# Optimization experiments

Hardware: AMD Instinct MI355X
Metric: run time of the kernel (lower is better)

The kernel has to match this reference:

```python
import jax, jax.numpy as jnp
import numpy as np

N_NODES = 50000
N_REL = 4
N_EDGES = 250000
IN_F, HID_F, OUT_F = 512, 512, 256


def setup_inputs() -> dict:
    key = jax.random.key(0)
    ks = jax.random.split(key, 9)
    x = jax.random.normal(ks[0], (N_NODES, IN_F), dtype=jnp.float32)
    edge_src = jax.random.randint(ks[1], (N_REL, N_EDGES), 0, N_NODES, dtype=jnp.int64)
    edge_dst = jax.random.randint(ks[2], (N_REL, N_EDGES), 0, N_NODES, dtype=jnp.int64)
    s1 = 1.0 / np.sqrt(IN_F)
    s2 = 1.0 / np.sqrt(HID_F)
    Wself1 = jax.random.normal(ks[3], (N_REL, IN_F, HID_F), dtype=jnp.float32) * s1
    Wneigh1 = jax.random.normal(ks[4], (N_REL, IN_F, HID_F), dtype=jnp.float32) * s1
    b1 = jnp.zeros((N_REL, HID_F), dtype=jnp.float32)
    Wself2 = jax.random.normal(ks[5], (N_REL, HID_F, OUT_F), dtype=jnp.float32) * s2
    Wneigh2 = jax.random.normal(ks[6], (N_REL, HID_F, OUT_F), dtype=jnp.float32) * s2
    b2 = jnp.zeros((N_REL, OUT_F), dtype=jnp.float32)
    return {"x": x, "Wself1": Wself1, "Wneigh1": Wneigh1, "b1": b1,
            "Wself2": Wself2, "Wneigh2": Wneigh2, "b2": b2,
            "edge_src": edge_src, "edge_dst": edge_dst}


def _hetero_sage_layer(h, Wself, Wneigh, b, edge_src, edge_dst):
    """HeteroGraphConv(sum) over per-relation SAGEConv(mean) layers.

    DGL SAGEConv(mean): out_r = h @ W_self_r + mean_in_neigh(h) @ W_neigh_r + b_r;
    zero-in-degree nodes get a zero neighbor term (divide by max(deg,1)).
    """
    n = h.shape[0]
    out = jnp.zeros((n, Wself.shape[-1]), dtype=h.dtype)
    for r in range(Wself.shape[0]):  # small fixed number of relations
        src, dst = edge_src[r], edge_dst[r]
        deg = jax.ops.segment_sum(jnp.ones(src.shape, dtype=h.dtype), dst, num_segments=n)
        neigh_sum = jax.ops.segment_sum(h[src], dst, num_segments=n)  # [n, d]
        neigh = neigh_sum / jnp.maximum(deg, 1.0)[:, None]
        out = out + h @ Wself[r] + neigh @ Wneigh[r] + b[r]
    return out


def reference(x, Wself1, Wneigh1, b1, Wself2, Wneigh2, b2, edge_src, edge_dst):
    h = _hetero_sage_layer(x, Wself1, Wneigh1, b1, edge_src, edge_dst)
    h = jax.nn.relu(h)
    return _hetero_sage_layer(h, Wself2, Wneigh2, b2, edge_src, edge_dst)
```

## Files before the change

### kernel.cpp

```cpp
#include <hip/hip_runtime.h>
#include <stdint.h>

#define NNODES 50000
#define NREL 4
#define NEDGES 250000
#define INF 512
#define HIDF 512
#define OUTF 256
#define KCAT 2560
#define SCANB 49

typedef unsigned short u16;
typedef u16 u16x8 __attribute__((ext_vector_type(8)));
typedef __bf16 bf16x8 __attribute__((ext_vector_type(8)));
typedef float f32x4 __attribute__((ext_vector_type(4)));

__device__ __forceinline__ float bf2f(u16 b) {
    unsigned u = ((unsigned)b) << 16;
    return __builtin_bit_cast(float, u);
}
__device__ __forceinline__ u16 f2bf(float f) {
    unsigned u = __builtin_bit_cast(unsigned, f);
    u = (u + 0x7fffu + ((u >> 16) & 1u)) >> 16;
    return (u16)u;
}

#define GLOAD_LDS16(gsrc, ldst)                                                  \
    __builtin_amdgcn_global_load_lds(                                            \
        (__attribute__((address_space(1))) void*)(gsrc),                         \
        (__attribute__((address_space(3))) void*)(ldst), 16, 0, 0)


__global__ void cast_bf16_kernel(const float* __restrict__ in, u16* __restrict__ out, long total) {
    long i = ((long)blockIdx.x * blockDim.x + threadIdx.x) * 8;
    long stride = (long)gridDim.x * blockDim.x * 8;
    for (; i + 7 < total; i += stride) {
        float4 v0 = *(const float4*)(in + i);
        float4 v1 = *(const float4*)(in + i + 4);
        u16x8 o;
        o[0] = f2bf(v0.x); o[1] = f2bf(v0.y); o[2] = f2bf(v0.z); o[3] = f2bf(v0.w);
        o[4] = f2bf(v1.x); o[5] = f2bf(v1.y); o[6] = f2bf(v1.z); o[7] = f2bf(v1.w);
        *(u16x8*)(out + i) = o;
    }
}

__global__ void prep_w_kernel(const float* __restrict__ Wself, const float* __restrict__ Wneigh,
                              u16* __restrict__ WT, int N) {
    int total = N * KCAT;
    for (int idx = blockIdx.x * blockDim.x + threadIdx.x; idx < total;
         idx += gridDim.x * blockDim.x) {
        int n = idx / KCAT;
        int kg = idx - n * KCAT;
        int s = kg >> 9;
        int k = kg & 511;
        float v;
        if (s == 0) {
            v = Wself[(size_t)k * N + n] + Wself[(size_t)(512 + k) * N + n] +
                Wself[(size_t)(1024 + k) * N + n] + Wself[(size_t)(1536 + k) * N + n];
        } else {
            v = Wneigh[((size_t)(s - 1) * 512 + k) * N + n];
        }
        WT[idx] = f2bf(v);
    }
}

__global__ void prep_bias_kernel(const float* __restrict__ b1, const float* __restrict__ b2,
                                 float* __restrict__ b1s, float* __restrict__ b2s) {
    int t = threadIdx.x;
    if (t < HIDF) b1s[t] = b1[t] + b1[HIDF + t] + b1[2 * HIDF + t] + b1[3 * HIDF + t];
    if (t < OUTF) b2s[t] = b2[t] + b2[OUTF + t] + b2[2 * OUTF + t] + b2[3 * OUTF + t];
}


__global__ void hist_kernel(const int* __restrict__ dst, int* __restrict__ deg) {
    int tot = NREL * NEDGES;
    for (int i = blockIdx.x * blockDim.x + threadIdx.x; i < tot; i += gridDim.x * blockDim.x) {
        int r = i / NEDGES;
        atomicAdd(&deg[r * NNODES + dst[i]], 1);
    }
}

__global__ __launch_bounds__(1024) void scan1_kernel(const int* __restrict__ deg,
                                                     int* __restrict__ rp, int* __restrict__ bsum) {
    int rel = blockIdx.x / SCANB, blk = blockIdx.x % SCANB;
    int i = blk * 1024 + threadIdx.x;
    int v = (i < NNODES) ? deg[rel * NNODES + i] : 0;
    __shared__ int wsum[16];
    int lane = threadIdx.x & 63, wid = threadIdx.x >> 6;
    int x = v;
#pragma unroll
    for (int off = 1; off < 64; off <<= 1) {
        int o = __shfl_up(x, off);
        if (lane >= off) x += o;
    }
    if (lane == 63) wsum[wid] = x;
    __syncthreads();
    if (wid == 0) {
        int s = (lane < 16) ? wsum[lane] : 0;
#pragma unroll
        for (int off = 1; off < 16; off <<= 1) {
            int o = __shfl_up(s, off);
            if (lane >= off) s += o;
        }
        if (lane < 16) wsum[lane] = s;
    }
    __syncthreads();
    int excl = (wid > 0 ? wsum[wid - 1] : 0) + x - v;
    if (i < NNODES) rp[rel * (NNODES + 1) + i] = excl;
    if (threadIdx.x == 1023) bsum[blockIdx.x] = excl + v;
}

__global__ void scan2_kernel(const int* __restrict__ bsum, int* __restrict__ bofs) {
    int r = threadIdx.x >> 6, lane = threadIdx.x & 63;
    int v = (lane < SCANB) ? bsum[r * SCANB + lane] : 0;
    int x = v;
#pragma unroll
    for (int off = 1; off < 64; off <<= 1) {
        int o = __shfl_up(x, off);
        if (lane >= off) x += o;
    }
    if (lane < SCANB) bofs[r * SCANB + lane] = x - v;
}

__global__ __launch_bounds__(1024) void scan3_kernel(int* __restrict__ rp, int* __restrict__ cur,
                                                     const int* __restrict__ bofs) {
    int rel = blockIdx.x / SCANB, blk = blockIdx.x % SCANB;
    int i = blk * 1024 + threadIdx.x;
    if (i < NNODES) {
        int v = rp[rel * (NNODES + 1) + i] + bofs[rel * SCANB + blk];
        rp[rel * (NNODES + 1) + i] = v;
        cur[rel * NNODES + i] = v;
        if (i == 0) rp[rel * (NNODES + 1) + NNODES] = NEDGES;
    }
}

__global__ void fill_kernel(const int* __restrict__ esrc, const int* __restrict__ edst,
                            int* __restrict__ cur, int* __restrict__ col) {
    int tot = NREL * NEDGES;
    for (int i = blockIdx.x * blockDim.x + threadIdx.x; i < tot; i += gridDim.x * blockDim.x) {
        int r = i / NEDGES;
        int d = edst[i];
        int pos = atomicAdd(&cur[r * NNODES + d], 1);
        col[r * NEDGES + pos] = esrc[i];
    }
}


__global__ __launch_bounds__(256) void aggregate_kernel(const u16* __restrict__ src,
                                                        const int* __restrict__ rp,
                                                        const int* __restrict__ col,
                                                        u16* __restrict__ out) {
    int node = blockIdx.x * 4 + (threadIdx.x >> 6);
    int rel = blockIdx.y;
    if (node >= NNODES) return;
    const int* r = rp + rel * (NNODES + 1);
    const int* cl = col + rel * NEDGES;
    int l = threadIdx.x & 63;
    int p0 = r[node], p1 = r[node + 1];
    float scale = (p1 > p0) ? 1.0f / (float)(p1 - p0) : 1.0f;
    float acc[8] = {0.f, 0.f, 0.f, 0.f, 0.f, 0.f, 0.f, 0.f};
    int e = p0;
    for (; e + 2 <= p1; e += 2) {
        int s0 = cl[e], s1 = cl[e + 1];
        u16x8 v0 = *(const u16x8*)(src + (size_t)s0 * 512 + l * 8);
        u16x8 v1 = *(const u16x8*)(src + (size_t)s1 * 512 + l * 8);
#pragma unroll
        for (int j = 0; j < 8; ++j) acc[j] += bf2f(v0[j]) + bf2f(v1[j]);
    }
    if (e < p1) {
        int s0 = cl[e];
        u16x8 v0 = *(const u16x8*)(src + (size_t)s0 * 512 + l * 8);
#pragma unroll
        for (int j = 0; j < 8; ++j) acc[j] += bf2f(v0[j]);
    }
    u16x8 o;
#pragma unroll
    for (int j = 0; j < 8; ++j) o[j] = f2bf(acc[j] * scale);
    *(u16x8*)(out + ((size_t)rel * NNODES + node) * 512 + l * 8) = o;
}


template <int N, int OUTMODE>
__global__ __launch_bounds__(256, 4) void gemm_kernel(
    const u16* __restrict__ A0, const u16* __restrict__ A1, const u16* __restrict__ A2,
    const u16* __restrict__ A3, const u16* __restrict__ A4, const u16* __restrict__ WT,
    const float* __restrict__ bias, void* __restrict__ outp, int M) {
    __shared__ u16 ldsA[128 * 64];
    __shared__ u16 ldsB[128 * 64];
    const int t = threadIdx.x;
    const int w = t >> 6, l = t & 63;
    const int wr = w >> 1, wc = w & 1;

    constexpr int ncol = N >> 7;
    const int nwg = gridDim.x * gridDim.y;
    const int orig = blockIdx.y * gridDim.x + blockIdx.x;
    const int q = nwg >> 3, rr = nwg & 7, xcd = orig & 7, loc = orig >> 3;
    const int v = (xcd < rr) ? xcd * (q + 1) + loc : rr * (q + 1) + (xcd - rr) * q + loc;
    const int rowBase = (v / ncol) * 128;
    const int colBase = (v % ncol) * 128;

    f32x4 acc[4][4] = {};

    const u16* const As[5] = {A0, A1, A2, A3, A4};
    const int sr = t >> 3;
    const int gp = t & 7;
    const int lr = l & 15, lg = l >> 4;

#pragma unroll
    for (int s = 0; s < 5; ++s) {
        const u16* __restrict__ Asrc = As[s];
        for (int ts = 0; ts < 8; ++ts) {
            const int klocal = ts * 64;
            const int kglob = s * 512 + klocal;
#pragma unroll
            for (int c = 0; c < 4; ++c) {
                int r = c * 32 + sr;
                int gl = gp ^ (r & 7);
                int grow = rowBase + r;
                if (grow > M - 1) grow = M - 1;
                const u16* gsrc = Asrc + (size_t)grow * 512 + klocal + gl * 8;
                GLOAD_LDS16(gsrc, ldsA + (c * 2048 + w * 512));
            }
#pragma unroll
            for (int c = 0; c < 4; ++c) {
                int r = c * 32 + sr;
                int gl = gp ^ (r & 7);
                const u16* gsrc = WT + (size_t)(colBase + r) * KCAT + kglob + gl * 8;
                GLOAD_LDS16(gsrc, ldsB + (c * 2048 + w * 512));
            }
            __syncthreads();
#pragma unroll
            for (int kh = 0; kh < 2; ++kh) {
                bf16x8 av[4], bv[4];
#pragma unroll
                for (int m = 0; m < 4; ++m) {
                    int r = wr * 64 + m * 16 + lr;
                    int g = (kh * 4 + lg) ^ (r & 7);
                    av[m] = *(const bf16x8*)((const char*)ldsA + r * 128 + g * 16);
                }
#pragma unroll
                for (int n = 0; n < 4; ++n) {
                    int r = wc * 64 + n * 16 + lr;
                    int g = (kh * 4 + lg) ^ (r & 7);
                    bv[n] = *(const bf16x8*)((const char*)ldsB + r * 128 + g * 16);
                }
#pragma unroll
                for (int m = 0; m < 4; ++m)
#pragma unroll
                    for (int n = 0; n < 4; ++n)
                        acc[m][n] =
                            __builtin_amdgcn_mfma_f32_16x16x32_bf16(av[m], bv[n], acc[m][n], 0, 0, 0);
            }
            __syncthreads();
        }
    }

    const int lq = l >> 4;
#pragma unroll
    for (int m = 0; m < 4; ++m) {
#pragma unroll
        for (int n = 0; n < 4; ++n) {
#pragma unroll
            for (int j = 0; j < 4; ++j) {
                int row = rowBase + wr * 64 + m * 16 + lq * 4 + j;
                int colc = colBase + wc * 64 + n * 16 + lr;
                if (row < M) {
                    float vv = acc[m][n][j] + bias[colc];
                    if (OUTMODE == 0) {
                        vv = vv > 0.f ? vv : 0.f;
                        ((u16*)outp)[(size_t)row * N + colc] = f2bf(vv);
                    } else {
                        ((float*)outp)[(size_t)row * N + colc] = vv;
                    }
                }
            }
        }
    }
}


extern "C" void kernel_launch(void* const* d_in, const int* in_sizes, int n_in,
                              void* d_out, int out_size, void* d_ws, size_t ws_size,
                              hipStream_t stream) {
    const float* x = (const float*)d_in[0];
    const float* Wself1 = (const float*)d_in[1];
    const float* Wneigh1 = (const float*)d_in[2];
    const float* b1 = (const float*)d_in[3];
    const float* Wself2 = (const float*)d_in[4];
    const float* Wneigh2 = (const float*)d_in[5];
    const float* b2 = (const float*)d_in[6];
    const int* esrc = (const int*)d_in[7];
    const int* edst = (const int*)d_in[8];

    char* ws = (char*)d_ws;
    size_t off = 0;
    auto alloc = [&](size_t bytes) {
        char* p = ws + off;
        off += (bytes + 255) & ~(size_t)255;
        return p;
    };
    const size_t plane = (size_t)NNODES * 512;
    u16* xB = (u16*)alloc(plane * 2);
    u16* mB = (u16*)alloc(NREL * plane * 2);
    u16* h1B = (u16*)alloc(plane * 2);
    u16* WT1 = (u16*)alloc((size_t)HIDF * KCAT * 2);
    u16* WT2 = (u16*)alloc((size_t)OUTF * KCAT * 2);
    float* b1s = (float*)alloc(HIDF * 4);
    float* b2s = (float*)alloc(OUTF * 4);
    int* deg = (int*)alloc((size_t)NREL * NNODES * 4);
    int* rp = (int*)alloc((size_t)NREL * (NNODES + 1) * 4);
    int* cur = (int*)alloc((size_t)NREL * NNODES * 4);
    int* col = (int*)alloc((size_t)NREL * NEDGES * 4);
    int* bsum = (int*)alloc((size_t)NREL * SCANB * 4);
    int* bofs = (int*)alloc((size_t)NREL * SCANB * 4);

    hipMemsetAsync(deg, 0, (size_t)NREL * NNODES * 4, stream);
    cast_bf16_kernel<<<12500, 256, 0, stream>>>(x, xB, (long)NNODES * INF);
    prep_w_kernel<<<1280, 256, 0, stream>>>(Wself1, Wneigh1, WT1, HIDF);
    prep_w_kernel<<<640, 256, 0, stream>>>(Wself2, Wneigh2, WT2, OUTF);
    prep_bias_kernel<<<1, 512, 0, stream>>>(b1, b2, b1s, b2s);
    hist_kernel<<<1024, 256, 0, stream>>>(edst, deg);
    scan1_kernel<<<NREL * SCANB, 1024, 0, stream>>>(deg, rp, bsum);
    scan2_kernel<<<1, 256, 0, stream>>>(bsum, bofs);
    scan3_kernel<<<NREL * SCANB, 1024, 0, stream>>>(rp, cur, bofs);
    fill_kernel<<<1024, 256, 0, stream>>>(esrc, edst, cur, col);

    aggregate_kernel<<<dim3(12500, 4), 256, 0, stream>>>(xB, rp, col, mB);
    gemm_kernel<HIDF, 0><<<dim3(4, 391), 256, 0, stream>>>(
        xB, mB, mB + plane, mB + 2 * plane, mB + 3 * plane, WT1, b1s, h1B, NNODES);

    aggregate_kernel<<<dim3(12500, 4), 256, 0, stream>>>(h1B, rp, col, mB);
    gemm_kernel<OUTF, 1><<<dim3(2, 391), 256, 0, stream>>>(
        h1B, mB, mB + plane, mB + 2 * plane, mB + 3 * plane, WT2, b2s, d_out, NNODES);
}
```

Baseline: 855.6 us.

## Merge weight/bias prep kernels, use 2D grids for CSR build, batch neighbor index loads

Fuses the two weight-prep launches and the bias-prep launch into one kernel to cut launch count. Histogram and fill kernels now use a 2D grid with one thread per edge instead of grid-stride loops with integer division. The aggregation kernel loads up to 64 neighbor indices per wavefront in one coalesced read, broadcasts them with readlane, and unrolls the gather by four for more memory-level parallelism. The aggregation is the main change; the cost is more register use and a slightly different float summation order.

Measured after the change: 867.5 us. About the same (+1.4%).

```diff
diff --git a/kernel.cpp b/kernel.cpp
--- a/kernel.cpp
+++ b/kernel.cpp
@@ -44,40 +44,50 @@
     }
 }
 
-__global__ void prep_w_kernel(const float* __restrict__ Wself, const float* __restrict__ Wneigh,
-                              u16* __restrict__ WT, int N) {
-    int total = N * KCAT;
+__global__ void prep_weights_kernel(const float* __restrict__ Ws1, const float* __restrict__ Wn1,
+                                    const float* __restrict__ Ws2, const float* __restrict__ Wn2,
+                                    const float* __restrict__ b1, const float* __restrict__ b2,
+                                    u16* __restrict__ WT1, u16* __restrict__ WT2,
+                                    float* __restrict__ b1s, float* __restrict__ b2s) {
+    const int T1 = HIDF * KCAT;
+    const int T2 = OUTF * KCAT;
+    const int total = T1 + T2 + HIDF + OUTF;
     for (int idx = blockIdx.x * blockDim.x + threadIdx.x; idx < total;
          idx += gridDim.x * blockDim.x) {
-        int n = idx / KCAT;
-        int kg = idx - n * KCAT;
-        int s = kg >> 9;
-        int k = kg & 511;
-        float v;
-        if (s == 0) {
-            v = Wself[(size_t)k * N + n] + Wself[(size_t)(512 + k) * N + n] +
-                Wself[(size_t)(1024 + k) * N + n] + Wself[(size_t)(1536 + k) * N + n];
+        if (idx < T1 + T2) {
+            const float* Wself;
+            const float* Wneigh;
+            u16* WT;
+            int N, id;
+            if (idx < T1) { Wself = Ws1; Wneigh = Wn1; WT = WT1; N = HIDF; id = idx; }
+            else          { Wself = Ws2; Wneigh = Wn2; WT = WT2; N = OUTF; id = idx - T1; }
+            int n = id / KCAT;
+            int kg = id - n * KCAT;
+            int s = kg >> 9;
+            int k = kg & 511;
+            float v;
+            if (s == 0) {
+                v = Wself[(size_t)k * N + n] + Wself[(size_t)(512 + k) * N + n] +
+                    Wself[(size_t)(1024 + k) * N + n] + Wself[(size_t)(1536 + k) * N + n];
+            } else {
+                v = Wneigh[((size_t)(s - 1) * 512 + k) * N + n];
+            }
+            WT[id] = f2bf(v);
+        } else if (idx < T1 + T2 + HIDF) {
+            int t = idx - T1 - T2;
+            b1s[t] = b1[t] + b1[HIDF + t] + b1[2 * HIDF + t] + b1[3 * HIDF + t];
         } else {
-            v = Wneigh[((size_t)(s - 1) * 512 + k) * N + n];
-        }
-        WT[idx] = f2bf(v);
-    }
-}
-
-__global__ void prep_bias_kernel(const float* __restrict__ b1, const float* __restrict__ b2,
-                                 float* __restrict__ b1s, float* __restrict__ b2s) {
-    int t = threadIdx.x;
-    if (t < HIDF) b1s[t] = b1[t] + b1[HIDF + t] + b1[2 * HIDF + t] + b1[3 * HIDF + t];
-    if (t < OUTF) b2s[t] = b2[t] + b2[OUTF + t] + b2[2 * OUTF + t] + b2[3 * OUTF + t];
+            int t = idx - T1 - T2 - HIDF;
+            b2s[t] = b2[t] + b2[OUTF + t] + b2[2 * OUTF + t] + b2[3 * OUTF + t];
+        }
+    }
 }
 
 
 __global__ void hist_kernel(const int* __restrict__ dst, int* __restrict__ deg) {
-    int tot = NREL * NEDGES;
-    for (int i = blockIdx.x * blockDim.x + threadIdx.x; i < tot; i += gridDim.x * blockDim.x) {
-        int r = i / NEDGES;
-        atomicAdd(&deg[r * NNODES + dst[i]], 1);
-    }
+    int r = blockIdx.y;
+    int i = blockIdx.x * blockDim.x + threadIdx.x;
+    if (i < NEDGES) atomicAdd(&deg[r * NNODES + dst[r * NEDGES + i]], 1);
 }
 
 __global__ __launch_bounds__(1024) void scan1_kernel(const int* __restrict__ deg,
@@ -136,12 +146,12 @@
 
 __global__ void fill_kernel(const int* __restrict__ esrc, const int* __restrict__ edst,
                             int* __restrict__ cur, int* __restrict__ col) {
-    int tot = NREL * NEDGES;
-    for (int i = blockIdx.x * blockDim.x + threadIdx.x; i < tot; i += gridDim.x * blockDim.x) {
-        int r = i / NEDGES;
-        int d = edst[i];
+    int r = blockIdx.y;
+    int i = blockIdx.x * blockDim.x + threadIdx.x;
+    if (i < NEDGES) {
+        int d = edst[r * NEDGES + i];
         int pos = atomicAdd(&cur[r * NNODES + d], 1);
-        col[r * NEDGES + pos] = esrc[i];
+        col[r * NEDGES + pos] = esrc[r * NEDGES + i];
     }
 }
 
@@ -157,21 +167,35 @@
     const int* cl = col + rel * NEDGES;
     int l = threadIdx.x & 63;
     int p0 = r[node], p1 = r[node + 1];
-    float scale = (p1 > p0) ? 1.0f / (float)(p1 - p0) : 1.0f;
+    int d = p1 - p0;
+    float scale = (d > 0) ? 1.0f / (float)d : 1.0f;
     float acc[8] = {0.f, 0.f, 0.f, 0.f, 0.f, 0.f, 0.f, 0.f};
-    int e = p0;
-    for (; e + 2 <= p1; e += 2) {
-        int s0 = cl[e], s1 = cl[e + 1];
-        u16x8 v0 = *(const u16x8*)(src + (size_t)s0 * 512 + l * 8);
-        u16x8 v1 = *(const u16x8*)(src + (size_t)s1 * 512 + l * 8);
-#pragma unroll
-        for (int j = 0; j < 8; ++j) acc[j] += bf2f(v0[j]) + bf2f(v1[j]);
-    }
-    if (e < p1) {
-        int s0 = cl[e];
-        u16x8 v0 = *(const u16x8*)(src + (size_t)s0 * 512 + l * 8);
-#pragma unroll
-        for (int j = 0; j < 8; ++j) acc[j] += bf2f(v0[j]);
+    const u16* srcl = src + l * 8;
+    for (int base = 0; base < d; base += 64) {
+        int ci = p0 + base + l;
+        int myc = cl[ci < p1 ? ci : (p1 - 1)];
+        int lim = d - base;
+        if (lim > 64) lim = 64;
+        int e = 0;
+        for (; e + 4 <= lim; e += 4) {
+            int s0 = __builtin_amdgcn_readlane(myc, e);
+            int s1 = __builtin_amdgcn_readlane(myc, e + 1);
+            int s2 = __builtin_amdgcn_readlane(myc, e + 2);
+            int s3 = __builtin_amdgcn_readlane(myc, e + 3);
+            u16x8 v0 = *(const u16x8*)(srcl + (size_t)s0 * 512);
+            u16x8 v1 = *(const u16x8*)(srcl + (size_t)s1 * 512);
+            u16x8 v2 = *(const u16x8*)(srcl + (size_t)s2 * 512);
+            u16x8 v3 = *(const u16x8*)(srcl + (size_t)s3 * 512);
+#pragma unroll
+            for (int j = 0; j < 8; ++j)
+                acc[j] += (bf2f(v0[j]) + bf2f(v1[j])) + (bf2f(v2[j]) + bf2f(v3[j]));
+        }
+        for (; e < lim; ++e) {
+            int s0 = __builtin_amdgcn_readlane(myc, e);
+            u16x8 v0 = *(const u16x8*)(srcl + (size_t)s0 * 512);
+#pragma unroll
+            for (int j = 0; j < 8; ++j) acc[j] += bf2f(v0[j]);
+        }
     }
     u16x8 o;
 #pragma unroll
@@ -316,14 +340,13 @@
 
     hipMemsetAsync(deg, 0, (size_t)NREL * NNODES * 4, stream);
     cast_bf16_kernel<<<12500, 256, 0, stream>>>(x, xB, (long)NNODES * INF);
-    prep_w_kernel<<<1280, 256, 0, stream>>>(Wself1, Wneigh1, WT1, HIDF);
-    prep_w_kernel<<<640, 256, 0, stream>>>(Wself2, Wneigh2, WT2, OUTF);
-    prep_bias_kernel<<<1, 512, 0, stream>>>(b1, b2, b1s, b2s);
-    hist_kernel<<<1024, 256, 0, stream>>>(edst, deg);
+    prep_weights_kernel<<<1920, 256, 0, stream>>>(Wself1, Wneigh1, Wself2, Wneigh2,
+                                                  b1, b2, WT1, WT2, b1s, b2s);
+    hist_kernel<<<dim3(977, 4), 256, 0, stream>>>(edst, deg);
     scan1_kernel<<<NREL * SCANB, 1024, 0, stream>>>(deg, rp, bsum);
     scan2_kernel<<<1, 256, 0, stream>>>(bsum, bofs);
     scan3_kernel<<<NREL * SCANB, 1024, 0, stream>>>(rp, cur, bofs);
-    fill_kernel<<<1024, 256, 0, stream>>>(esrc, edst, cur, col);
+    fill_kernel<<<dim3(977, 4), 256, 0, stream>>>(esrc, edst, cur, col);
 
     aggregate_kernel<<<dim3(12500, 4), 256, 0, stream>>>(xB, rp, col, mB);
     gemm_kernel<HIDF, 0><<<dim3(4, 391), 256, 0, stream>>>(
```
